# Optimization experiments

Hardware: AMD Instinct MI355X
Metric: run time of the kernel (lower is better)

The kernel has to match this reference:

```python
import jax, jax.numpy as jnp
import numpy as np

B, L, D, H = 2, 2048, 1024, 16
HD = D // H
EPS = 1e-6

def _rms(x, w):
    return x * jax.lax.rsqrt(jnp.mean(x * x, axis=-1, keepdims=True) + EPS) * w

def _lin(x, w, b=None):
    y = x @ w.T
    return y if b is None else y + b

def setup_inputs() -> dict:
    key = jax.random.key(0)
    ks = jax.random.split(key, 16)
    def w(i, shape, s=0.02):
        return jax.random.normal(ks[i], shape, dtype=jnp.float32) * s
    return dict(
        z=jax.random.normal(ks[0], (B, L, D), dtype=jnp.float32),
        connection=jax.random.normal(ks[1], (B, L, D), dtype=jnp.float32),
        w_z=jnp.ones(D, jnp.float32), w_c=jnp.ones(D, jnp.float32), w_mlp=jnp.ones(D, jnp.float32),
        f_w1=w(2, (2 * D, D)), f_b1=jnp.zeros(2 * D, jnp.float32),
        f_w2=w(3, (D, 2 * D)), f_b2=jnp.zeros(D, jnp.float32),
        g_w1=w(4, (D, 2 * D)), g_b1=jnp.zeros(D, jnp.float32),
        g_w2=w(5, (D, D)), g_b2=jnp.zeros(D, jnp.float32),
        dt=jnp.float32(0.1),
        q_w=w(6, (D, 2 * D)), k_w=w(7, (D, 2 * D)), v_w=w(8, (D, D)), o_w=w(9, (D, D)),
        temp=jnp.float32(1.0),
        cu_w1=w(10, (2 * D, 3 * D)), cu_b1=jnp.zeros(2 * D, jnp.float32),
        cu_w2=w(11, (D, 2 * D)), cu_b2=jnp.zeros(D, jnp.float32),
        m_w1=w(12, (4 * D, D)), m_b1=jnp.zeros(4 * D, jnp.float32),
        m_w2=w(13, (D, 4 * D)), m_b2=jnp.zeros(D, jnp.float32),
    )

def reference(z, connection, w_z, w_c, w_mlp,
              f_w1, f_b1, f_w2, f_b2, g_w1, g_b1, g_w2, g_b2, dt,
              q_w, k_w, v_w, o_w, temp,
              cu_w1, cu_b1, cu_w2, cu_b2,
              m_w1, m_b1, m_w2, m_b2):
    z_before = z
    zn = _rms(z, w_z)
    cn = _rms(connection, w_c)

    # covariant vector field: dz = dt * (F(zn) + gamma(cat(cn, F(zn))))
    dz_local = _lin(jax.nn.silu(_lin(zn, f_w1, f_b1)), f_w2, f_b2)
    corr = _lin(jnp.tanh(_lin(jnp.concatenate([cn, dz_local], -1), g_w1, g_b1)), g_w2, g_b2)
    dz = dt * (dz_local + corr)

    # covariant sigmoid attention
    zc = jnp.concatenate([zn, cn], -1)                       # [B,L,2D]
    Q = _lin(zc, q_w).reshape(B, L, H, HD).transpose(0, 2, 1, 3)  # bhld
    K = _lin(zc, k_w).reshape(B, L, H, HD).transpose(0, 2, 1, 3)
    V = _lin(zn, v_w).reshape(B, L, H, HD).transpose(0, 2, 1, 3)
    scores = jnp.einsum('bhld,bhmd->bhlm', Q, K) * (HD ** -0.5) * temp
    rel = jax.nn.sigmoid(scores)
    rel_sum = jnp.clip(jnp.sum(rel, -1, keepdims=True), 1.0, None)
    attn = jnp.einsum('bhlm,bhmd->bhld', rel, V) / rel_sum
    ctx = _lin(attn.transpose(0, 2, 1, 3).reshape(B, L, D), o_w)

    z1 = z + dz + ctx

    # connection update
    delta = _lin(jax.nn.silu(_lin(jnp.concatenate([connection, z1, dz], -1), cu_w1, cu_b1)), cu_w2, cu_b2)
    conn_new = connection + delta

    # MLP block
    z2 = z1 + _lin(jax.nn.silu(_lin(_rms(z1, w_mlp), m_w1, m_b1)), m_w2, m_b2)
    return (z2, conn_new, z_before)
```

## Files before the change

kernel.cpp:

```cpp
#include <hip/hip_runtime.h>


typedef unsigned short u16;
typedef __attribute__((ext_vector_type(8))) short short8;
typedef __attribute__((ext_vector_type(8))) unsigned short us8;
typedef __attribute__((ext_vector_type(4))) float f32x4;
typedef __attribute__((ext_vector_type(4))) unsigned short us4;
typedef __attribute__((ext_vector_type(2))) unsigned int u32x2;

__device__ __forceinline__ float b2f(u16 u) {
    union { unsigned u; float f; } c; c.u = ((unsigned)u) << 16; return c.f;
}
__device__ __forceinline__ u16 f2b(float f) {
    union { float f; unsigned u; } c; c.f = f;
    unsigned x = c.u;
    unsigned r = (x + 0x7fffu + ((x >> 16) & 1u)) >> 16;
    return (u16)r;
}
__device__ __forceinline__ float fast_rcp(float x) {
    return __builtin_amdgcn_rcpf(x);
}
__device__ __forceinline__ unsigned cvt_pk_bf16(float a, float b) {
    unsigned r;
    asm("v_cvt_pk_bf16_f32 %0, %1, %2" : "=v"(r) : "v"(a), "v"(b));
    return r;
}

__device__ __forceinline__ void async_copy16(const u16* g, u16* l) {
    __builtin_amdgcn_global_load_lds(
        (const __attribute__((address_space(1))) unsigned int*)(g),
        (__attribute__((address_space(3))) unsigned int*)(l), 16, 0, 0);
}

__global__ __launch_bounds__(256) void cvt_k(const float* __restrict__ s,
                                             u16* __restrict__ d, int n) {
    int i = (blockIdx.x * 256 + threadIdx.x) * 4;
    if (i >= n) return;
    f32x4 v = *(const f32x4*)(s + i);
    us4 o;
#pragma unroll
    for (int k = 0; k < 4; k++) o[k] = f2b(v[k]);
    *(us4*)(d + i) = o;
}

__global__ __launch_bounds__(256) void rmsf_k(const float* __restrict__ x,
                                              const float* __restrict__ w,
                                              u16* __restrict__ y,
                                              float* __restrict__ cp, int D) {
    int n = blockIdx.x;
    const float* xr = x + (size_t)n * D;
    int i0 = threadIdx.x << 2;
    f32x4 v = *(const f32x4*)(xr + i0);
    if (cp) *(f32x4*)(cp + (size_t)n * D + i0) = v;
    float s = v[0] * v[0] + v[1] * v[1] + v[2] * v[2] + v[3] * v[3];
#pragma unroll
    for (int m = 32; m >= 1; m >>= 1) s += __shfl_xor(s, m, 64);
    __shared__ float red[4];
    if ((threadIdx.x & 63) == 0) red[threadIdx.x >> 6] = s;
    __syncthreads();
    float tot = red[0] + red[1] + red[2] + red[3];
    float scale = rsqrtf(tot / (float)D + 1e-6f);
    f32x4 wv = *(const f32x4*)(w + i0);
    us4 o;
#pragma unroll
    for (int k = 0; k < 4; k++) o[k] = f2b(v[k] * scale * wv[k]);
    *(us4*)(y + (size_t)n * D + i0) = o;
}

__global__ __launch_bounds__(256) void rmsb_k(const u16* __restrict__ x,
                                              const float* __restrict__ w,
                                              u16* __restrict__ y, int D) {
    int n = blockIdx.x;
    const u16* xr = x + (size_t)n * D;
    int i0 = threadIdx.x << 2;
    us4 xv = *(const us4*)(xr + i0);
    float v[4]; float s = 0.f;
#pragma unroll
    for (int k = 0; k < 4; k++) { v[k] = b2f(xv[k]); s += v[k] * v[k]; }
#pragma unroll
    for (int m = 32; m >= 1; m >>= 1) s += __shfl_xor(s, m, 64);
    __shared__ float red[4];
    if ((threadIdx.x & 63) == 0) red[threadIdx.x >> 6] = s;
    __syncthreads();
    float tot = red[0] + red[1] + red[2] + red[3];
    float scale = rsqrtf(tot / (float)D + 1e-6f);
    f32x4 wv = *(const f32x4*)(w + i0);
    us4 o;
#pragma unroll
    for (int k = 0; k < 4; k++) o[k] = f2b(v[k] * scale * wv[k]);
    *(us4*)(y + (size_t)n * D + i0) = o;
}

template <int BN, int NSEG>
__global__ __launch_bounds__(256) void gemm_t(const u16* __restrict__ A0,
                                              const u16* __restrict__ A1,
                                              const u16* __restrict__ A2,
                                              const u16* __restrict__ W,
                                              const float* __restrict__ bias,
                                              u16* __restrict__ C,
                                              int K, int O, int act, int mode) {
    constexpr int NJ = BN / 32;
    constexpr int WN = BN / 2;
    __shared__ u16 Asm[2][128 * 64];
    __shared__ u16 Bsm[2][BN * 64];

    const int tid = threadIdx.x;
    const int wid = tid >> 6, lane = tid & 63;
    const int l15 = lane & 15, quad = lane >> 4;
    const int lsw = l15 & 7;
    const int row0 = blockIdx.y * 128, col0 = blockIdx.x * BN;
    const int wm = (wid >> 1) << 6, wn = (wid & 1) * WN;

    const int rb = tid >> 3;
    const int gg = ((tid & 7) ^ (rb & 7)) << 3;
    const int sA = (NSEG == 1) ? K : 1024;
    const size_t aoff = (size_t)(row0 + rb) * sA + gg;
    const size_t boff = (size_t)(col0 + rb) * K + gg;
    const int ldsb = wid << 9;

    f32x4 acc[4][NJ];
#pragma unroll
    for (int i = 0; i < 4; i++)
#pragma unroll
        for (int j = 0; j < NJ; j++) acc[i][j] = (f32x4){0.f, 0.f, 0.f, 0.f};

    auto stage = [&](int buf, int kof) {
        const u16* Ab; int kcol;
        if constexpr (NSEG == 1) { Ab = A0; kcol = kof; }
        else {
            int seg = kof >> 10;
            Ab = (seg == 0) ? A0 : ((NSEG == 3 && seg == 2) ? A2 : A1);
            kcol = kof & 1023;
        }
        const u16* as = Ab + aoff + kcol;
        const u16* bs = W + boff + kof;
#pragma unroll
        for (int i = 0; i < 4; i++)
            async_copy16(as + (size_t)(32 * i) * sA, &Asm[buf][(i << 11) + ldsb]);
#pragma unroll
        for (int i = 0; i < BN / 32; i++)
            async_copy16(bs + (size_t)(32 * i) * K, &Bsm[buf][(i << 11) + ldsb]);
    };

    const int nk = K >> 6;
    stage(0, 0);
    __syncthreads();
    for (int kk = 0; kk < nk; kk++) {
        int cur = kk & 1;
        if (kk + 1 < nk) stage(1 - cur, (kk + 1) << 6);
        const u16* Ab = Asm[cur];
        const u16* Bb = Bsm[cur];
#pragma unroll
        for (int h = 0; h < 2; h++) {
            const int gq = (((h << 2) + quad) ^ lsw) << 3;
            short8 af[4], bf[NJ];
#pragma unroll
            for (int i = 0; i < 4; i++)
                af[i] = *(const short8*)&Ab[(wm + i * 16 + l15) * 64 + gq];
#pragma unroll
            for (int j = 0; j < NJ; j++)
                bf[j] = *(const short8*)&Bb[(wn + j * 16 + l15) * 64 + gq];
#pragma unroll
            for (int i = 0; i < 4; i++)
#pragma unroll
                for (int j = 0; j < NJ; j++)
                    acc[i][j] = __builtin_amdgcn_mfma_f32_16x16x32_bf16(af[i], bf[j], acc[i][j], 0, 0, 0);
        }
        __syncthreads();
    }

    if (mode == 0) {
#pragma unroll
        for (int j = 0; j < NJ; j++) {
            int col = col0 + wn + j * 16 + l15;
            float bb = bias ? bias[col] : 0.f;
#pragma unroll
            for (int i = 0; i < 4; i++) {
                int rowb = row0 + wm + i * 16 + (quad << 2);
#pragma unroll
                for (int g = 0; g < 4; g++) {
                    float v = acc[i][j][g] + bb;
                    if (act == 1) {
                        v = v * fast_rcp(1.f + __expf(-v));
                    } else if (act == 2) {
                        float t = __expf(v * 2.f);
                        v = 1.f - 2.f * fast_rcp(1.f + t);
                    }
                    C[(size_t)(rowb + g) * O + col] = f2b(v);
                }
            }
        }
    } else {
#pragma unroll
        for (int j = 0; j < NJ; j++) {
            int col = col0 + wn + j * 16 + l15;
            int h = col >> 6, d = col & 63;
#pragma unroll
            for (int i = 0; i < 4; i++) {
                int rowb = row0 + wm + i * 16 + (quad << 2);
                int bb_ = rowb >> 11;
                int tok = rowb & 2047;
                us4 pk;
#pragma unroll
                for (int g = 0; g < 4; g++) pk[g] = f2b(acc[i][j][g]);
                *(us4*)&C[(size_t)(((bb_ << 4) + h) * 64 + d) * 2048 + tok] = pk;
            }
        }
    }
}

__global__ __launch_bounds__(256) void attn_k(const u16* __restrict__ QK,
                                              const u16* __restrict__ VT,
                                              const float* __restrict__ temp_p,
                                              u16* __restrict__ Oa) {
    const int L = 2048, D = 1024, SQ = 2048;
    __shared__ u16 Ks[2][64 * 64];
    __shared__ u16 Vs[2][64 * 64];
    __shared__ u16 plds[4][16 * 72];

    const int tid = threadIdx.x;
    const int w = tid >> 6, lane = tid & 63;
    const int l15 = lane & 15, quad = lane >> 4;
    const int bh = blockIdx.x >> 4;
    const int qb0 = (blockIdx.x & 15) << 7;
    const int b = bh >> 4, h = bh & 15;
    const float nsc2 = -0.125f * temp_p[0] * 1.44269504f;

    short8 aq[2][2];
#pragma unroll
    for (int qt = 0; qt < 2; qt++) {
        size_t row = (size_t)(b * L + qb0 + w * 32 + qt * 16 + l15) * SQ + h * 64;
#pragma unroll
        for (int hf = 0; hf < 2; hf++)
            aq[qt][hf] = *(const short8*)(QK + row + hf * 32 + quad * 8);
    }

    const u16* Kbase = QK + 1024 + (size_t)(b * L) * SQ + h * 64;
    const u16* VTb   = VT + (size_t)bh * 64 * L;

    const int i0 = tid, i1 = tid + 256;
    const int r0 = i0 >> 3, g0 = (i0 & 7) ^ (r0 & 7);
    const int r1 = i1 >> 3, g1 = (i1 & 7) ^ (r1 & 7);
    const u16* kS0 = Kbase + (size_t)r0 * SQ + g0 * 8;
    const u16* kS1 = Kbase + (size_t)r1 * SQ + g1 * 8;
    const u16* vS0 = VTb + (size_t)r0 * L + g0 * 8;
    const u16* vS1 = VTb + (size_t)r1 * L + g1 * 8;

    auto stage = [&](int buf, int mc) {
        async_copy16(kS0 + (size_t)mc * SQ, &Ks[buf][w << 9]);
        async_copy16(kS1 + (size_t)mc * SQ, &Ks[buf][2048 + (w << 9)]);
        async_copy16(vS0 + mc, &Vs[buf][w << 9]);
        async_copy16(vS1 + mc, &Vs[buf][2048 + (w << 9)]);
    };

    f32x4 acc[2][4];
#pragma unroll
    for (int i = 0; i < 2; i++)
#pragma unroll
        for (int j = 0; j < 4; j++) acc[i][j] = (f32x4){0.f, 0.f, 0.f, 0.f};
    float rs[2] = {0.f, 0.f};
    u16* P = plds[w];
    const int lsw = l15 & 7;

    stage(0, 0);
    __syncthreads();
    for (int it = 0; it < 32; it++) {
        int cur = it & 1;
        if (it < 31) stage(1 - cur, (it + 1) << 6);
        const u16* Kt = Ks[cur];
        const u16* Vt = Vs[cur];
#pragma unroll
        for (int qt = 0; qt < 2; qt++) {
#pragma unroll
            for (int ks = 0; ks < 4; ks++) {
                f32x4 s = (f32x4){0.f, 0.f, 0.f, 0.f};
#pragma unroll
                for (int hf = 0; hf < 2; hf++) {
                    int slot = ((ks * 16 + l15) * 8 + ((hf * 4 + quad) ^ lsw)) * 8;
                    short8 bk = *(const short8*)&Kt[slot];
                    s = __builtin_amdgcn_mfma_f32_16x16x32_bf16(bk, aq[qt][hf], s, 0, 0, 0);
                }
                float p0 = fast_rcp(1.f + __builtin_amdgcn_exp2f(s[0] * nsc2));
                float p1 = fast_rcp(1.f + __builtin_amdgcn_exp2f(s[1] * nsc2));
                float p2 = fast_rcp(1.f + __builtin_amdgcn_exp2f(s[2] * nsc2));
                float p3 = fast_rcp(1.f + __builtin_amdgcn_exp2f(s[3] * nsc2));
                rs[qt] += (p0 + p1) + (p2 + p3);
                u32x2 pk2;
                pk2[0] = cvt_pk_bf16(p0, p1);
                pk2[1] = cvt_pk_bf16(p2, p3);
                *(u32x2*)&P[l15 * 72 + ks * 16 + (quad << 2)] = pk2;
            }
#pragma unroll
            for (int kh = 0; kh < 2; kh++) {
                short8 ap = *(const short8*)&P[l15 * 72 + kh * 32 + quad * 8];
#pragma unroll
                for (int dt = 0; dt < 4; dt++) {
                    int slot = ((dt * 16 + l15) * 8 + ((kh * 4 + quad) ^ lsw)) * 8;
                    short8 bv = *(const short8*)&Vt[slot];
                    acc[qt][dt] = __builtin_amdgcn_mfma_f32_16x16x32_bf16(ap, bv, acc[qt][dt], 0, 0, 0);
                }
            }
        }
        __syncthreads();
    }

#pragma unroll
    for (int qt = 0; qt < 2; qt++) {
        rs[qt] += __shfl_xor(rs[qt], 16, 64);
        rs[qt] += __shfl_xor(rs[qt], 32, 64);
    }

#pragma unroll
    for (int qt = 0; qt < 2; qt++) {
        u16* orow = Oa + (size_t)(b * L + qb0 + w * 32 + qt * 16) * D + h * 64;
#pragma unroll
        for (int g = 0; g < 4; g++) {
            int row = quad * 4 + g;
            float denom = __shfl(rs[qt], row, 64);
            float rd = fast_rcp(fmaxf(denom, 1.0f));
#pragma unroll
            for (int dt = 0; dt < 4; dt++)
                orow[(size_t)row * D + dt * 16 + l15] = f2b(acc[qt][dt][g] * rd);
        }
    }
}

__global__ void dz_k(u16* __restrict__ d, const u16* __restrict__ a,
                     const u16* __restrict__ b, const float* __restrict__ dtp, int n) {
    int i = (blockIdx.x * 256 + threadIdx.x) * 8;
    if (i >= n) return;
    float dt = dtp[0];
    us8 va = *(const us8*)(a + i), vb = *(const us8*)(b + i);
    us8 o;
#pragma unroll
    for (int k = 0; k < 8; k++) o[k] = f2b(dt * (b2f(va[k]) + b2f(vb[k])));
    *(us8*)(d + i) = o;
}

__global__ void z1_k(u16* __restrict__ d, const float* __restrict__ z,
                     const u16* __restrict__ dz, const u16* __restrict__ ctx, int n) {
    int i = (blockIdx.x * 256 + threadIdx.x) * 8;
    if (i >= n) return;
    f32x4 z0 = *(const f32x4*)(z + i), z4 = *(const f32x4*)(z + i + 4);
    us8 vd = *(const us8*)(dz + i), vc = *(const us8*)(ctx + i);
    us8 o;
#pragma unroll
    for (int k = 0; k < 4; k++) {
        o[k]     = f2b(z0[k] + b2f(vd[k])     + b2f(vc[k]));
        o[k + 4] = f2b(z4[k] + b2f(vd[k + 4]) + b2f(vc[k + 4]));
    }
    *(us8*)(d + i) = o;
}

__global__ void connew_k(float* __restrict__ d, const float* __restrict__ conn,
                         const u16* __restrict__ delta, int n) {
    int i = (blockIdx.x * 256 + threadIdx.x) * 8;
    if (i >= n) return;
    f32x4 c0 = *(const f32x4*)(conn + i), c4 = *(const f32x4*)(conn + i + 4);
    us8 vd = *(const us8*)(delta + i);
    f32x4 o0, o4;
#pragma unroll
    for (int k = 0; k < 4; k++) {
        o0[k] = c0[k] + b2f(vd[k]);
        o4[k] = c4[k] + b2f(vd[k + 4]);
    }
    *(f32x4*)(d + i) = o0;
    *(f32x4*)(d + i + 4) = o4;
}

__global__ void z2_k(float* __restrict__ d, const u16* __restrict__ z1,
                     const u16* __restrict__ mf, int n) {
    int i = (blockIdx.x * 256 + threadIdx.x) * 8;
    if (i >= n) return;
    us8 va = *(const us8*)(z1 + i), vb = *(const us8*)(mf + i);
    f32x4 o0, o4;
#pragma unroll
    for (int k = 0; k < 4; k++) {
        o0[k] = b2f(va[k]) + b2f(vb[k]);
        o4[k] = b2f(va[k + 4]) + b2f(vb[k + 4]);
    }
    *(f32x4*)(d + i) = o0;
    *(f32x4*)(d + i + 4) = o4;
}

extern "C" void kernel_launch(void* const* d_in, const int* in_sizes, int n_in,
                              void* d_out, int out_size, void* d_ws, size_t ws_size,
                              hipStream_t stream) {
    const int B = 2, L = 2048, D = 1024, H = 16, N = B * L;
    const float* z      = (const float*)d_in[0];
    const float* conn   = (const float*)d_in[1];
    const float* w_z    = (const float*)d_in[2];
    const float* w_c    = (const float*)d_in[3];
    const float* w_mlp  = (const float*)d_in[4];
    const float* f_w1   = (const float*)d_in[5];
    const float* f_b1   = (const float*)d_in[6];
    const float* f_w2   = (const float*)d_in[7];
    const float* f_b2   = (const float*)d_in[8];
    const float* g_w1   = (const float*)d_in[9];
    const float* g_b1   = (const float*)d_in[10];
    const float* g_w2   = (const float*)d_in[11];
    const float* g_b2   = (const float*)d_in[12];
    const float* dt_p   = (const float*)d_in[13];
    const float* q_w    = (const float*)d_in[14];
    const float* k_w    = (const float*)d_in[15];
    const float* v_w    = (const float*)d_in[16];
    const float* o_w    = (const float*)d_in[17];
    const float* temp_p = (const float*)d_in[18];
    const float* cu_w1  = (const float*)d_in[19];
    const float* cu_b1  = (const float*)d_in[20];
    const float* cu_w2  = (const float*)d_in[21];
    const float* cu_b2  = (const float*)d_in[22];
    const float* m_w1   = (const float*)d_in[23];
    const float* m_b1   = (const float*)d_in[24];
    const float* m_w2   = (const float*)d_in[25];
    const float* m_b2   = (const float*)d_in[26];

    float* out = (float*)d_out;
    u16* ws  = (u16*)d_ws;
    const size_t U = (size_t)N * D;

    u16* zn    = ws + 0 * U;
    u16* cn    = ws + 1 * U;
    u16* h1    = ws + 2 * U;
    u16* dzl   = ws + 4 * U;
    u16* gh    = ws + 5 * U;
    u16* corr  = ws + 6 * U;
    u16* dz    = ws + 7 * U;
    u16* connb = ws + 8 * U;
    u16* QK    = ws + 2 * U;
    u16* VT    = ws + 4 * U;
    u16* attnb = ws + 1 * U;
    u16* ctx   = ws + 4 * U;
    u16* z1    = ws + 5 * U;
    u16* cu_h  = ws + 2 * U;
    u16* delta = ws + 1 * U;
    u16* z1n   = ws + 0 * U;
    u16* mh    = ws + 1 * U;
    u16* mf    = ws + 6 * U;

    u16* wb = ws + 9 * U;
    u16* bf_w1  = wb + 0;
    u16* bf_w2  = wb + 2 * 1024 * 1024;
    u16* bg_w1  = wb + 4 * 1024 * 1024;
    u16* bg_w2  = wb + 6 * 1024 * 1024;
    u16* bqk_w  = wb + 7 * 1024 * 1024;
    u16* bv_w   = wb + 11 * 1024 * 1024;
    u16* bo_w   = wb + 12 * 1024 * 1024;
    u16* bcu_w1 = wb + 13 * 1024 * 1024;
    u16* bcu_w2 = wb + 19 * 1024 * 1024;
    u16* bm_w1  = wb + 21 * 1024 * 1024;
    u16* bm_w2  = wb + 25 * 1024 * 1024;

    auto cvt = [&](const float* s, u16* d, int n) {
        cvt_k<<<n / 1024, 256, 0, stream>>>(s, d, n);
    };
    cvt(f_w1, bf_w1, 2 * D * D);   cvt(f_w2, bf_w2, 2 * D * D);
    cvt(g_w1, bg_w1, 2 * D * D);   cvt(g_w2, bg_w2, D * D);
    cvt(q_w, bqk_w, 2 * D * D);    cvt(k_w, bqk_w + 2 * D * D, 2 * D * D);
    cvt(v_w, bv_w, D * D);         cvt(o_w, bo_w, D * D);
    cvt(cu_w1, bcu_w1, 6 * D * D); cvt(cu_w2, bcu_w2, 2 * D * D);
    cvt(m_w1, bm_w1, 4 * D * D);   cvt(m_w2, bm_w2, 4 * D * D);
    cvt(conn, connb, N * D);

    const int EW8 = (N * D / 8 + 255) / 256;
    auto gemm = [&](const u16* A, const u16* W, const float* bias, u16* C,
                    int K, int O, int act, int mode = 0) {
        if (O == 1024) {
            dim3 grid(16, 32);
            gemm_t<64, 1><<<grid, 256, 0, stream>>>(A, nullptr, nullptr, W, bias, C, K, O, act, mode);
        } else {
            dim3 grid(O / 128, 32);
            gemm_t<128, 1><<<grid, 256, 0, stream>>>(A, nullptr, nullptr, W, bias, C, K, O, act, mode);
        }
    };

    rmsf_k<<<N, 256, 0, stream>>>(z, w_z, zn, out + 2 * U, D);
    rmsf_k<<<N, 256, 0, stream>>>(conn, w_c, cn, nullptr, D);

    gemm(zn, bf_w1, f_b1, h1, D, 2 * D, 1);
    gemm(h1, bf_w2, f_b2, dzl, 2 * D, D, 0);
    gemm_t<64, 2><<<dim3(16, 32), 256, 0, stream>>>(
        cn, dzl, nullptr, bg_w1, g_b1, gh, 2 * D, D, 2, 0);
    gemm(gh, bg_w2, g_b2, corr, D, D, 0);
    dz_k<<<EW8, 256, 0, stream>>>(dz, dzl, corr, dt_p, N * D);

    gemm_t<128, 2><<<dim3(16, 32), 256, 0, stream>>>(
        zn, cn, nullptr, bqk_w, nullptr, QK, 2 * D, 2 * D, 0, 0);
    gemm(zn, bv_w, nullptr, VT, D, D, 0, 1);
    attn_k<<<B * H * L / 128, 256, 0, stream>>>(QK, VT, temp_p, attnb);
    gemm(attnb, bo_w, nullptr, ctx, D, D, 0);

    z1_k<<<EW8, 256, 0, stream>>>(z1, z, dz, ctx, N * D);

    gemm_t<128, 3><<<dim3(16, 32), 256, 0, stream>>>(
        connb, z1, dz, bcu_w1, cu_b1, cu_h, 3 * D, 2 * D, 1, 0);
    gemm(cu_h, bcu_w2, cu_b2, delta, 2 * D, D, 0);
    connew_k<<<EW8, 256, 0, stream>>>(out + U, conn, delta, N * D);

    rmsb_k<<<N, 256, 0, stream>>>(z1, w_mlp, z1n, D);
    gemm(z1n, bm_w1, m_b1, mh, D, 4 * D, 1);
    gemm(mh, bm_w2, m_b2, mf, 4 * D, D, 0);
    z2_k<<<EW8, 256, 0, stream>>>(out, z1, mf, N * D);
}
```

Before: 749.9 us.

## Swizzle workgroup IDs across XCDs, fuse connection cast into RMS norm

Remaps block IDs in the GEMM and attention kernels so consecutive blocks are spread round-robin over the 8 XCDs, which is meant to improve L2 locality for tiles that share operands. Folds the fp32-to-bf16 conversion of the connection tensor into the RMS-norm kernel that already reads it, removing a separate launch and one full read pass. Also uses packed bf16 conversion instructions in the transposed GEMM epilogue. The remap assumes the grid size is a multiple of 8.

```diff
diff --git a/kernel.cpp b/kernel.cpp
--- a/kernel.cpp
+++ b/kernel.cpp
@@ -46,12 +46,19 @@
 __global__ __launch_bounds__(256) void rmsf_k(const float* __restrict__ x,
                                               const float* __restrict__ w,
                                               u16* __restrict__ y,
-                                              float* __restrict__ cp, int D) {
+                                              float* __restrict__ cp,
+                                              u16* __restrict__ cb, int D) {
     int n = blockIdx.x;
     const float* xr = x + (size_t)n * D;
     int i0 = threadIdx.x << 2;
     f32x4 v = *(const f32x4*)(xr + i0);
     if (cp) *(f32x4*)(cp + (size_t)n * D + i0) = v;
+    if (cb) {
+        us4 o2;
+#pragma unroll
+        for (int k = 0; k < 4; k++) o2[k] = f2b(v[k]);
+        *(us4*)(cb + (size_t)n * D + i0) = o2;
+    }
     float s = v[0] * v[0] + v[1] * v[1] + v[2] * v[2] + v[3] * v[3];
 #pragma unroll
     for (int m = 32; m >= 1; m >>= 1) s += __shfl_xor(s, m, 64);
@@ -108,7 +115,13 @@
     const int wid = tid >> 6, lane = tid & 63;
     const int l15 = lane & 15, quad = lane >> 4;
     const int lsw = l15 & 7;
-    const int row0 = blockIdx.y * 128, col0 = blockIdx.x * BN;
+
+    const int nwg = gridDim.x * gridDim.y;
+    int id = blockIdx.y * gridDim.x + blockIdx.x;
+    id = (id & 7) * (nwg >> 3) + (id >> 3);
+    const int bx = id % gridDim.x, by = id / gridDim.x;
+
+    const int row0 = by * 128, col0 = bx * BN;
     const int wm = (wid >> 1) << 6, wn = (wid & 1) * WN;
 
     const int rb = tid >> 3;
@@ -200,10 +213,10 @@
                 int rowb = row0 + wm + i * 16 + (quad << 2);
                 int bb_ = rowb >> 11;
                 int tok = rowb & 2047;
-                us4 pk;
-#pragma unroll
-                for (int g = 0; g < 4; g++) pk[g] = f2b(acc[i][j][g]);
-                *(us4*)&C[(size_t)(((bb_ << 4) + h) * 64 + d) * 2048 + tok] = pk;
+                u32x2 pk2;
+                pk2[0] = cvt_pk_bf16(acc[i][j][0], acc[i][j][1]);
+                pk2[1] = cvt_pk_bf16(acc[i][j][2], acc[i][j][3]);
+                *(u32x2*)&C[(size_t)(((bb_ << 4) + h) * 64 + d) * 2048 + tok] = pk2;
             }
         }
     }
@@ -221,8 +234,10 @@
     const int tid = threadIdx.x;
     const int w = tid >> 6, lane = tid & 63;
     const int l15 = lane & 15, quad = lane >> 4;
-    const int bh = blockIdx.x >> 4;
-    const int qb0 = (blockIdx.x & 15) << 7;
+    int id = blockIdx.x;
+    id = (id & 7) * 64 + (id >> 3);
+    const int bh = id >> 4;
+    const int qb0 = (id & 15) << 7;
     const int b = bh >> 4, h = bh & 15;
     const float nsc2 = -0.125f * temp_p[0] * 1.44269504f;
 
@@ -460,7 +475,6 @@
     cvt(v_w, bv_w, D * D);         cvt(o_w, bo_w, D * D);
     cvt(cu_w1, bcu_w1, 6 * D * D); cvt(cu_w2, bcu_w2, 2 * D * D);
     cvt(m_w1, bm_w1, 4 * D * D);   cvt(m_w2, bm_w2, 4 * D * D);
-    cvt(conn, connb, N * D);
 
     const int EW8 = (N * D / 8 + 255) / 256;
     auto gemm = [&](const u16* A, const u16* W, const float* bias, u16* C,
@@ -474,8 +488,8 @@
         }
     };
 
-    rmsf_k<<<N, 256, 0, stream>>>(z, w_z, zn, out + 2 * U, D);
-    rmsf_k<<<N, 256, 0, stream>>>(conn, w_c, cn, nullptr, D);
+    rmsf_k<<<N, 256, 0, stream>>>(z, w_z, zn, out + 2 * U, nullptr, D);
+    rmsf_k<<<N, 256, 0, stream>>>(conn, w_c, cn, nullptr, connb, D);
 
     gemm(zn, bf_w1, f_b1, h1, D, 2 * D, 1);
     gemm(h1, bf_w2, f_b2, dzl, 2 * D, D, 0);
```

Measured after the change: 729.9 us. 1.03x faster.
